# Optimization experiments

Hardware: AMD Instinct MI355X
Metric: run time of the kernel (lower is better)

Reference implementation:

```python
import jax, jax.numpy as jnp
import numpy as np

# batch, net nodes/graph, vnr nodes/graph, hidden, static feats, vnr feats, vnf types, value out
B, NN, NV, H, FS, FV, T, O = 64, 1000, 10, 128, 8, 6, 8, 64
EN, EV = B * NN * 8, B * NV * 4  # total edges (avg degree 8 / 4)


def _gat(h, src, dst, W, al, ar, b):
    """dgl GATConv, num_heads=1, activation=None, allow_zero_in_degree=True."""
    n = h.shape[0]
    z = h @ W                                                    # [N,H]
    e = jax.nn.leaky_relu((z @ al)[src] + (z @ ar)[dst], 0.2)    # [E]
    emax = jax.ops.segment_max(e, dst, num_segments=n)
    ee = jnp.exp(e - emax[dst])
    alpha = ee / jax.ops.segment_sum(ee, dst, num_segments=n)[dst]
    return jax.ops.segment_sum(z[src] * alpha[:, None], dst, num_segments=n) + b


def _gru_cell(x, h, W_ih, W_hh, b_ih, b_hh):
    gi = x @ W_ih.T + b_ih
    gh = h @ W_hh.T + b_hh
    ir, iz, in_ = jnp.split(gi, 3, axis=-1)
    hr, hz, hn = jnp.split(gh, 3, axis=-1)
    r = jax.nn.sigmoid(ir + hr)
    z = jax.nn.sigmoid(iz + hz)
    n = jnp.tanh(in_ + r * hn)
    return (1.0 - z) * n + z * h


def _forward(static_feat, vnr_feat, nmask,
             Ws1, als1, ars1, bs1, Ws2, als2, ars2, bs2, Ws3, als3, ars3, bs3,
             Wv1, alv1, arv1, bv1, Wv2, alv2, arv2, bv2, Wv3, alv3, arv3, bv3,
             W_attn, v_attn, W_ih, W_hh, b_ih, b_hh, h0, W_out, b_out,
             src_s, dst_s, src_v, dst_v, vnr_VNF, net_VNF):
    # ---- graph encoders: 3 stacked GAT layers each ----
    hs = _gat(static_feat, src_s, dst_s, Ws1, als1, ars1, bs1)
    hs = _gat(hs, src_s, dst_s, Ws2, als2, ars2, bs2)
    hs = _gat(hs, src_s, dst_s, Ws3, als3, ars3, bs3)            # [B*NN,H]
    hv = _gat(vnr_feat, src_v, dst_v, Wv1, alv1, arv1, bv1)
    hv = _gat(hv, src_v, dst_v, Wv2, alv2, arv2, bv2)
    hv = _gat(hv, src_v, dst_v, Wv3, alv3, arv3, bv3)            # [B*NV,H]
    static_hidden = hs.reshape(B, NN, H).transpose(0, 2, 1)      # [B,H,NN]
    vnr_hidden = hv.reshape(B, NV, H).transpose(0, 2, 1)         # [B,H,NV]

    # ---- pointer decoder ----
    netV = net_VNF.reshape(B, NN, T)
    # mask[b,i,n] = netV[b, n, vnr_VNF[b,i]]
    masks = jnp.take_along_axis(netV[:, None, :, :], vnr_VNF[:, :, None, None], axis=3)[..., 0]  # [B,NV,NN]

    def step(h, x):
        h_new = _gru_cell(x, h, W_ih, W_hh, b_ih, b_hh)          # [B,H]
        cat = jnp.concatenate(
            [static_hidden, jnp.broadcast_to(h_new[:, :, None], (B, H, NN))], axis=1)  # [B,2H,NN]
        attn = jnp.einsum('h,bhn->bn', v_attn,
                          jnp.tanh(jnp.einsum('hk,bkn->bhn', W_attn, cat)))
        return h_new, attn

    h0b = jnp.broadcast_to(h0, (B, H))
    xs = vnr_hidden.transpose(2, 0, 1)                            # [NV,B,H]
    _, attns = jax.lax.scan(step, h0b, xs)                        # [NV,B,NN]
    pi = (attns.transpose(1, 0, 2) + jnp.log(masks.astype(jnp.float32))).reshape(B, -1)

    # ---- value head ----
    nm = nmask.reshape(B, NV)
    y1 = (vnr_hidden.transpose(0, 2, 1) * nm[:, :, None]).sum(1) / nm.sum(1, keepdims=True)
    y2 = static_hidden.mean(2)
    val = jnp.concatenate([y1, y2], axis=1) @ W_out.T + b_out     # [B,O]
    return pi, val


def setup_inputs() -> dict:
    key = jax.random.key(0)
    ks = iter(jax.random.split(key, 60))

    def nrm(shape, fan):
        return jax.random.normal(next(ks), shape, jnp.float32) / np.sqrt(fan).astype(np.float32)

    inp = {
        'static_feat': jax.random.normal(next(ks), (B * NN, FS), jnp.float32),
        'vnr_feat': jax.random.normal(next(ks), (B * NV, FV), jnp.float32),
        'nmask': jnp.ones((B * NV,), jnp.float32),
    }
    for pfx, fin in (('s1', FS), ('s2', H), ('s3', H), ('v1', FV), ('v2', H), ('v3', H)):
        inp['W' + pfx] = nrm((fin, H), fin)
        inp['al' + pfx] = nrm((H,), H)
        inp['ar' + pfx] = nrm((H,), H)
        inp['b' + pfx] = jnp.zeros((H,), jnp.float32)
    inp['W_attn'] = nrm((H, 2 * H), 2 * H)
    inp['v_attn'] = nrm((H,), H)
    inp['W_ih'] = nrm((3 * H, H), H)
    inp['W_hh'] = nrm((3 * H, H), H)
    inp['b_ih'] = jnp.zeros((3 * H,), jnp.float32)
    inp['b_hh'] = jnp.zeros((3 * H,), jnp.float32)
    inp['h0'] = jnp.zeros((H,), jnp.float32)
    inp['W_out'] = nrm((O, 2 * H), 2 * H)
    inp['b_out'] = jnp.zeros((O,), jnp.float32)
    inp['src_s'] = jax.random.randint(next(ks), (EN,), 0, B * NN)
    inp['dst_s'] = jax.random.randint(next(ks), (EN,), 0, B * NN)
    inp['src_v'] = jax.random.randint(next(ks), (EV,), 0, B * NV)
    inp['dst_v'] = jax.random.randint(next(ks), (EV,), 0, B * NV)
    inp['vnr_VNF'] = jax.random.randint(next(ks), (B, NV), 0, T)
    inp['net_VNF'] = jnp.ones((B * NN, T), jnp.int32)
    return inp


def reference(static_feat, vnr_feat, nmask,
              Ws1, als1, ars1, bs1, Ws2, als2, ars2, bs2, Ws3, als3, ars3, bs3,
              Wv1, alv1, arv1, bv1, Wv2, alv2, arv2, bv2, Wv3, alv3, arv3, bv3,
              W_attn, v_attn, W_ih, W_hh, b_ih, b_hh, h0, W_out, b_out,
              src_s, dst_s, src_v, dst_v, vnr_VNF, net_VNF):
    return _forward(static_feat, vnr_feat, nmask,
                    Ws1, als1, ars1, bs1, Ws2, als2, ars2, bs2, Ws3, als3, ars3, bs3,
                    Wv1, alv1, arv1, bv1, Wv2, alv2, arv2, bv2, Wv3, alv3, arv3, bv3,
                    W_attn, v_attn, W_ih, W_hh, b_ih, b_hh, h0, W_out, b_out,
                    src_s, dst_s, src_v, dst_v, vnr_VNF, net_VNF)
```

## Files before the change

kernel.cpp:

```cpp
#include <hip/hip_runtime.h>
#include <hip/hip_bf16.h>
#include <math.h>

#define B_   64
#define NN_  1000
#define NV_  10
#define H_   128
#define FS_  8
#define FV_  6
#define T_   8
#define O_   64
#define EN_  512000
#define EV_  2560
#define NS_  (B_*NN_)
#define NVT_ (B_*NV_)
#define RNG_S (NS_/8)
#define RNG_V (NVT_/8)

typedef __attribute__((ext_vector_type(8))) short short8v;
typedef __attribute__((ext_vector_type(4))) float floatx4;

__device__ __forceinline__ float fast_rcp(float x) { return __builtin_amdgcn_rcpf(x); }
__device__ __forceinline__ float fast_tanh(float x) {
  return 1.f - 2.f*fast_rcp(1.f + __expf(2.f*x));
}
__device__ __forceinline__ float fast_sigmoid(float x) {
  return fast_rcp(1.f + __expf(-x));
}
__device__ __forceinline__ unsigned short bf16_rne(float x) {
  unsigned u = __float_as_uint(x);
  return (unsigned short)((u + 0x7FFFu + ((u >> 16) & 1u)) >> 16);
}
__device__ __forceinline__ float bf16_tof(unsigned short b) {
  return __uint_as_float(((unsigned)b) << 16);
}
__device__ __forceinline__ float dot4(float4 a, float4 b) {
  return a.x*b.x + a.y*b.y + a.z*b.z + a.w*b.w;
}
__device__ __forceinline__ float lrelu02(float e) {
  return (e > 0.f) ? e : 0.2f*e;
}

__global__ __launch_bounds__(256) void k_count_r(const int* __restrict__ dst_s,
                                                 const int* __restrict__ dst_v,
                                                 int* __restrict__ counts_s,
                                                 int* __restrict__ counts_v) {
  int bid = blockIdx.x;
  int r = bid & 7;
  int i = (bid >> 3)*256 + threadIdx.x;
  if (i < EN_) {
    int d = dst_s[i];
    int lo = r*RNG_S;
    if (d >= lo && d < lo + RNG_S) atomicAdd(&counts_s[d], 1);
  } else if (i < EN_ + EV_) {
    int d = dst_v[i - EN_];
    int lo = r*RNG_V;
    if (d >= lo && d < lo + RNG_V) atomicAdd(&counts_v[d], 1);
  }
}

__global__ __launch_bounds__(256) void k_scan_local(const int* cnt, int n, int* out, int* bsum) {
  __shared__ int s[256];
  int t = threadIdx.x; int i = blockIdx.x*256 + t;
  int v = (i < n) ? cnt[i] : 0;
  s[t] = v; __syncthreads();
  #pragma unroll
  for (int o = 1; o < 256; o <<= 1) {
    int u = (t >= o) ? s[t-o] : 0; __syncthreads();
    s[t] += u; __syncthreads();
  }
  if (i < n) out[i] = s[t] - v;
  if (t == 255) bsum[blockIdx.x] = s[255];
}

__global__ __launch_bounds__(1024) void k_scan_small(int* bsum, int nb,
                                                     const int* cntv, int* rowptr_v, int nv) {
  __shared__ int sums[1024];
  int t = threadIdx.x;
  if (blockIdx.x == 0) {
    int v = (t < nb) ? bsum[t] : 0;
    sums[t] = v; __syncthreads();
    for (int o = 1; o < 1024; o <<= 1) {
      int u = (t >= o) ? sums[t-o] : 0; __syncthreads();
      sums[t] += u; __syncthreads();
    }
    if (t < nb) bsum[t] = sums[t] - v;
  } else {
    int v = (t < nv) ? cntv[t] : 0;
    sums[t] = v; __syncthreads();
    for (int o = 1; o < 1024; o <<= 1) {
      int u = (t >= o) ? sums[t-o] : 0; __syncthreads();
      sums[t] += u; __syncthreads();
    }
    if (t < nv) rowptr_v[t] = sums[t] - v;
    if (t == nv-1) rowptr_v[nv] = sums[t];
  }
}

__global__ __launch_bounds__(256) void k_scan_add(int* out, const int* bsum, int n, int E) {
  int i = blockIdx.x*256 + threadIdx.x;
  if (i < n) out[i] += bsum[blockIdx.x];
  if (i == 0) out[n] = E;
}

__global__ __launch_bounds__(256) void k_scatter_r(const int* __restrict__ src_s,
                                                   const int* __restrict__ dst_s,
                                                   const int* __restrict__ src_v,
                                                   const int* __restrict__ dst_v,
                                                   const int* __restrict__ rowptr_s,
                                                   const int* __restrict__ rowptr_v,
                                                   int* __restrict__ cursor_s,
                                                   int* __restrict__ cursor_v,
                                                   unsigned short* __restrict__ srcp_s,
                                                   unsigned short* __restrict__ srcp_v) {
  int bid = blockIdx.x;
  int r = bid & 7;
  int i = (bid >> 3)*256 + threadIdx.x;
  if (i < EN_) {
    int d = dst_s[i];
    int lo = r*RNG_S;
    if (d >= lo && d < lo + RNG_S) {
      int pos = rowptr_s[d] + atomicAdd(&cursor_s[d], 1);
      srcp_s[pos] = (unsigned short)src_s[i];
    }
  } else if (i < EN_ + EV_) {
    int j = i - EN_;
    int d = dst_v[j];
    int lo = r*RNG_V;
    if (d >= lo && d < lo + RNG_V) {
      int pos = rowptr_v[d] + atomicAdd(&cursor_v[d], 1);
      srcp_v[pos] = (unsigned short)src_v[j];
    }
  }
}

__global__ __launch_bounds__(256) void k_prep(const float* W_ih, const float* Ws2,
                                              const float* Ws3, const float* W_attn,
                                              const float* Wv2, const float* Wv3,
                                              float* WTih,
                                              unsigned short* WS2hi, unsigned short* WS2lo,
                                              unsigned short* WS3hi, unsigned short* WS3lo,
                                              unsigned short* WAhi, unsigned short* WAlo,
                                              unsigned short* WV2hi, unsigned short* WV2lo,
                                              unsigned short* WV3hi, unsigned short* WV3lo) {
  int idx = blockIdx.x*256 + threadIdx.x;
  int task = blockIdx.y;
  if (task == 0) {
    if (idx < 128*384) {
      int k = idx / 384, j = idx - k*384;
      WTih[idx] = W_ih[(size_t)j*128 + k];
    }
  } else {
    if (idx >= 128*128) return;
    int j = idx >> 7, k = idx & 127;
    float v; unsigned short *hi, *lo;
    if (task == 1)      { v = Ws2[(size_t)k*128 + j];    hi = WS2hi; lo = WS2lo; }
    else if (task == 2) { v = Ws3[(size_t)k*128 + j];    hi = WS3hi; lo = WS3lo; }
    else if (task == 3) { v = W_attn[(size_t)j*256 + k]; hi = WAhi;  lo = WAlo;  }
    else if (task == 4) { v = Wv2[(size_t)k*128 + j];    hi = WV2hi; lo = WV2lo; }
    else                { v = Wv3[(size_t)k*128 + j];    hi = WV3hi; lo = WV3lo; }
    unsigned short h = bf16_rne(v);
    hi[idx] = h; lo[idx] = bf16_rne(v - bf16_tof(h));
  }
}

__global__ __launch_bounds__(256) void k_aggregate_split(int nNodes, const int* __restrict__ rowptr,
    const unsigned short* __restrict__ srcp, const float* __restrict__ el, const float* __restrict__ er,
    const unsigned short* __restrict__ z, const float* __restrict__ bias,
    unsigned short* __restrict__ outHi, unsigned short* __restrict__ outLo) {
  int w = (blockIdx.x*256 + threadIdx.x) >> 6;
  int lane = threadIdx.x & 63;
  if (w >= nNodes) return;
  int beg = rowptr[w], end = rowptr[w+1];
  float erw = er[w];
  float a0 = 0.f, a1 = 0.f, wsum = 0.f;
  for (int i = beg; i < end; i += 8) {
    int sI[8]; float lv[8]; ushort2 q[8];
    #pragma unroll
    for (int u = 0; u < 8; ++u) {
      int idx = i + u; idx = (idx < end) ? idx : (end - 1);
      sI[u] = srcp[idx];
    }
    #pragma unroll
    for (int u = 0; u < 8; ++u) lv[u] = el[sI[u]];
    #pragma unroll
    for (int u = 0; u < 8; ++u) q[u] = *(const ushort2*)(z + (size_t)sI[u]*H_ + lane*2);
    #pragma unroll
    for (int u = 0; u < 8; ++u) {
      float wt = (i + u < end) ? __expf(lrelu02(lv[u] + erw)) : 0.f;
      a0 += wt*bf16_tof(q[u].x);
      a1 += wt*bf16_tof(q[u].y);
      wsum += wt;
    }
  }
  float inv = (end > beg) ? fast_rcp(wsum) : 0.f;
  float o0 = a0*inv + bias[lane*2];
  float o1 = a1*inv + bias[lane*2 + 1];
  unsigned short h0 = bf16_rne(o0), h1 = bf16_rne(o1);
  ushort2 hv; hv.x = h0; hv.y = h1;
  ushort2 lv2; lv2.x = bf16_rne(o0 - bf16_tof(h0)); lv2.y = bf16_rne(o1 - bf16_tof(h1));
  *(ushort2*)(outHi + (size_t)w*H_ + lane*2) = hv;
  *(ushort2*)(outLo + (size_t)w*H_ + lane*2) = lv2;
}

__global__ __launch_bounds__(256) void k_mfma_gemm(
    const unsigned short* __restrict__ Ahi, const unsigned short* __restrict__ Alo,
    const unsigned short* __restrict__ WThi, const unsigned short* __restrict__ WTlo,
    float* __restrict__ C, unsigned short* __restrict__ Cb,
    const float* __restrict__ al, const float* __restrict__ ar,
    float* __restrict__ el, float* __restrict__ er) {
  __shared__ unsigned short lAhi[64*136];
  __shared__ unsigned short lAlo[64*136];
  __shared__ float redl[4][64];
  __shared__ float redr[4][64];
  int t = threadIdx.x;
  int row0 = blockIdx.x * 64;
  int wid = t >> 6, lane = t & 63;
  int g = lane >> 4, c = lane & 15;

  #pragma unroll
  for (int i = 0; i < 4; ++i) {
    int m = t + 256*i;
    int r = m >> 4;
    int kc = (m & 15) * 8;
    *(short8v*)(lAhi + r*136 + kc) = *(const short8v*)(Ahi + (size_t)(row0 + r)*H_ + kc);
    *(short8v*)(lAlo + r*136 + kc) = *(const short8v*)(Alo + (size_t)(row0 + r)*H_ + kc);
  }

  short8v bhi[2][4], blo[2][4];
  #pragma unroll
  for (int ct = 0; ct < 2; ++ct) {
    int col = wid*32 + ct*16 + c;
    #pragma unroll
    for (int kb = 0; kb < 4; ++kb) {
      size_t o = (size_t)col*H_ + kb*32 + g*8;
      bhi[ct][kb] = *(const short8v*)(WThi + o);
      blo[ct][kb] = *(const short8v*)(WTlo + o);
    }
  }

  floatx4 acc[4][2];
  #pragma unroll
  for (int rt = 0; rt < 4; ++rt)
    #pragma unroll
    for (int ct = 0; ct < 2; ++ct)
      acc[rt][ct] = (floatx4){0.f, 0.f, 0.f, 0.f};

  __syncthreads();

  #pragma unroll
  for (int kb = 0; kb < 4; ++kb) {
    short8v ahi[4], alo[4];
    #pragma unroll
    for (int rt = 0; rt < 4; ++rt) {
      int r = rt*16 + c;
      ahi[rt] = *(const short8v*)(lAhi + r*136 + kb*32 + g*8);
      alo[rt] = *(const short8v*)(lAlo + r*136 + kb*32 + g*8);
    }
    #pragma unroll
    for (int rt = 0; rt < 4; ++rt)
      #pragma unroll
      for (int ct = 0; ct < 2; ++ct) {
        acc[rt][ct] = __builtin_amdgcn_mfma_f32_16x16x32_bf16(ahi[rt], bhi[ct][kb], acc[rt][ct], 0, 0, 0);
        acc[rt][ct] = __builtin_amdgcn_mfma_f32_16x16x32_bf16(alo[rt], bhi[ct][kb], acc[rt][ct], 0, 0, 0);
        acc[rt][ct] = __builtin_amdgcn_mfma_f32_16x16x32_bf16(ahi[rt], blo[ct][kb], acc[rt][ct], 0, 0, 0);
      }
  }

  #pragma unroll
  for (int rt = 0; rt < 4; ++rt)
    #pragma unroll
    for (int i = 0; i < 4; ++i) {
      int row = row0 + rt*16 + g*4 + i;
      if (Cb) {
        unsigned short* cr = Cb + (size_t)row*H_ + wid*32;
        cr[c]      = bf16_rne(acc[rt][0][i]);
        cr[16 + c] = bf16_rne(acc[rt][1][i]);
      } else {
        float* cr = C + (size_t)row*H_ + wid*32;
        cr[c]      = acc[rt][0][i];
        cr[16 + c] = acc[rt][1][i];
      }
    }

  if (el) {
    float av0 = al[wid*32 + c], av1 = al[wid*32 + 16 + c];
    float rv0 = ar[wid*32 + c], rv1 = ar[wid*32 + 16 + c];
    #pragma unroll
    for (int rt = 0; rt < 4; ++rt)
      #pragma unroll
      for (int i = 0; i < 4; ++i) {
        float pl = acc[rt][0][i]*av0 + acc[rt][1][i]*av1;
        float pr = acc[rt][0][i]*rv0 + acc[rt][1][i]*rv1;
        pl += __shfl_xor(pl, 1, 64); pl += __shfl_xor(pl, 2, 64);
        pl += __shfl_xor(pl, 4, 64); pl += __shfl_xor(pl, 8, 64);
        pr += __shfl_xor(pr, 1, 64); pr += __shfl_xor(pr, 2, 64);
        pr += __shfl_xor(pr, 4, 64); pr += __shfl_xor(pr, 8, 64);
        if (c == 0) { redl[wid][rt*16 + g*4 + i] = pl; redr[wid][rt*16 + g*4 + i] = pr; }
      }
    __syncthreads();
    if (t < 64) {
      el[row0 + t] = redl[0][t] + redl[1][t] + redl[2][t] + redl[3][t];
      er[row0 + t] = redr[0][t] + redr[1][t] + redr[2][t] + redr[3][t];
    }
  }
}

__global__ __launch_bounds__(256) void k_agg_mfma(
    const int* __restrict__ rowptr, const unsigned short* __restrict__ srcp,
    const float* __restrict__ el_in, const float* __restrict__ er_in,
    const unsigned short* __restrict__ z_in, const float* __restrict__ bias,
    const unsigned short* __restrict__ WThi, const unsigned short* __restrict__ WTlo,
    unsigned short* __restrict__ zb_out, float* __restrict__ Cf,
    const float* __restrict__ al, const float* __restrict__ ar,
    float* __restrict__ el_out, float* __restrict__ er_out) {
  __shared__ unsigned short lAhi[64*136];
  __shared__ unsigned short lAlo[64*136];
  __shared__ float redl[4][64];
  __shared__ float redr[4][64];
  int t = threadIdx.x;
  int row0 = blockIdx.x * 64;
  int wid = t >> 6, lane = t & 63;
  int g = lane >> 4, c = lane & 15;

  float b0 = bias[lane*2], b1 = bias[lane*2 + 1];

  for (int j = 0; j < 8; ++j) {
    int wA = row0 + wid*16 + 2*j;
    int wB = wA + 1;
    int begA = rowptr[wA], endA = rowptr[wA+1];
    int begB = rowptr[wB], endB = rowptr[wB+1];
    float erA = er_in[wA], erB = er_in[wB];
    float a0A = 0.f, a1A = 0.f, wsA = 0.f;
    float a0B = 0.f, a1B = 0.f, wsB = 0.f;
    int iA = begA, iB = begB;
    while (iA < endA || iB < endB) {
      int sA[8], sB[8];
      #pragma unroll
      for (int u = 0; u < 8; ++u) {
        sA[u] = (iA + u < endA) ? (int)srcp[iA + u] : 0;
        sB[u] = (iB + u < endB) ? (int)srcp[iB + u] : 0;
      }
      float lA[8], lB[8];
      #pragma unroll
      for (int u = 0; u < 8; ++u) { lA[u] = el_in[sA[u]]; lB[u] = el_in[sB[u]]; }
      ushort2 qA[8], qB[8];
      #pragma unroll
      for (int u = 0; u < 8; ++u) {
        qA[u] = *(const ushort2*)(z_in + (size_t)sA[u]*H_ + lane*2);
        qB[u] = *(const ushort2*)(z_in + (size_t)sB[u]*H_ + lane*2);
      }
      #pragma unroll
      for (int u = 0; u < 8; ++u) {
        float wtA = (iA + u < endA) ? __expf(lrelu02(lA[u] + erA)) : 0.f;
        float wtB = (iB + u < endB) ? __expf(lrelu02(lB[u] + erB)) : 0.f;
        a0A += wtA*bf16_tof(qA[u].x); a1A += wtA*bf16_tof(qA[u].y); wsA += wtA;
        a0B += wtB*bf16_tof(qB[u].x); a1B += wtB*bf16_tof(qB[u].y); wsB += wtB;
      }
      iA += 8; iB += 8;
    }
    float invA = (endA > begA) ? fast_rcp(wsA) : 0.f;
    float invB = (endB > begB) ? fast_rcp(wsB) : 0.f;
    float o0A = a0A*invA + b0, o1A = a1A*invA + b1;
    float o0B = a0B*invB + b0, o1B = a1B*invB + b1;
    int rA = wid*16 + 2*j;
    unsigned short hA0 = bf16_rne(o0A), hA1 = bf16_rne(o1A);
    unsigned short hB0 = bf16_rne(o0B), hB1 = bf16_rne(o1B);
    ushort2 hvA; hvA.x = hA0; hvA.y = hA1;
    ushort2 lvA; lvA.x = bf16_rne(o0A - bf16_tof(hA0)); lvA.y = bf16_rne(o1A - bf16_tof(hA1));
    ushort2 hvB; hvB.x = hB0; hvB.y = hB1;
    ushort2 lvB; lvB.x = bf16_rne(o0B - bf16_tof(hB0)); lvB.y = bf16_rne(o1B - bf16_tof(hB1));
    *(ushort2*)(lAhi + rA*136 + lane*2) = hvA;
    *(ushort2*)(lAlo + rA*136 + lane*2) = lvA;
    *(ushort2*)(lAhi + (rA+1)*136 + lane*2) = hvB;
    *(ushort2*)(lAlo + (rA+1)*136 + lane*2) = lvB;
  }

  short8v bhi[2][4], blo[2][4];
  #pragma unroll
  for (int ct = 0; ct < 2; ++ct) {
    int col = wid*32 + ct*16 + c;
    #pragma unroll
    for (int kb = 0; kb < 4; ++kb) {
      size_t o = (size_t)col*H_ + kb*32 + g*8;
      bhi[ct][kb] = *(const short8v*)(WThi + o);
      blo[ct][kb] = *(const short8v*)(WTlo + o);
    }
  }

  floatx4 acc[4][2];
  #pragma unroll
  for (int rt = 0; rt < 4; ++rt)
    #pragma unroll
    for (int ct = 0; ct < 2; ++ct)
      acc[rt][ct] = (floatx4){0.f, 0.f, 0.f, 0.f};

  __syncthreads();

  #pragma unroll
  for (int kb = 0; kb < 4; ++kb) {
    short8v ahi[4], alo[4];
    #pragma unroll
    for (int rt = 0; rt < 4; ++rt) {
      int r = rt*16 + c;
      ahi[rt] = *(const short8v*)(lAhi + r*136 + kb*32 + g*8);
      alo[rt] = *(const short8v*)(lAlo + r*136 + kb*32 + g*8);
    }
    #pragma unroll
    for (int rt = 0; rt < 4; ++rt)
      #pragma unroll
      for (int ct = 0; ct < 2; ++ct) {
        acc[rt][ct] = __builtin_amdgcn_mfma_f32_16x16x32_bf16(ahi[rt], bhi[ct][kb], acc[rt][ct], 0, 0, 0);
        acc[rt][ct] = __builtin_amdgcn_mfma_f32_16x16x32_bf16(alo[rt], bhi[ct][kb], acc[rt][ct], 0, 0, 0);
        acc[rt][ct] = __builtin_amdgcn_mfma_f32_16x16x32_bf16(ahi[rt], blo[ct][kb], acc[rt][ct], 0, 0, 0);
      }
  }

  #pragma unroll
  for (int rt = 0; rt < 4; ++rt)
    #pragma unroll
    for (int i = 0; i < 4; ++i) {
      int row = row0 + rt*16 + g*4 + i;
      if (zb_out) {
        unsigned short* cr = zb_out + (size_t)row*H_ + wid*32;
        cr[c]      = bf16_rne(acc[rt][0][i]);
        cr[16 + c] = bf16_rne(acc[rt][1][i]);
      } else {
        float* cr = Cf + (size_t)row*H_ + wid*32;
        cr[c]      = acc[rt][0][i];
        cr[16 + c] = acc[rt][1][i];
      }
    }

  if (el_out) {
    float av0 = al[wid*32 + c], av1 = al[wid*32 + 16 + c];
    float rv0 = ar[wid*32 + c], rv1 = ar[wid*32 + 16 + c];
    #pragma unroll
    for (int rt = 0; rt < 4; ++rt)
      #pragma unroll
      for (int i = 0; i < 4; ++i) {
        float pl = acc[rt][0][i]*av0 + acc[rt][1][i]*av1;
        float pr = acc[rt][0][i]*rv0 + acc[rt][1][i]*rv1;
        pl += __shfl_xor(pl, 1, 64); pl += __shfl_xor(pl, 2, 64);
        pl += __shfl_xor(pl, 4, 64); pl += __shfl_xor(pl, 8, 64);
        pr += __shfl_xor(pr, 1, 64); pr += __shfl_xor(pr, 2, 64);
        pr += __shfl_xor(pr, 4, 64); pr += __shfl_xor(pr, 8, 64);
        if (c == 0) { redl[wid][rt*16 + g*4 + i] = pl; redr[wid][rt*16 + g*4 + i] = pr; }
      }
    __syncthreads();
    if (t < 64) {
      el_out[row0 + t] = redl[0][t] + redl[1][t] + redl[2][t] + redl[3][t];
      er_out[row0 + t] = redr[0][t] + redr[1][t] + redr[2][t] + redr[3][t];
    }
  }
}

__global__ __launch_bounds__(256) void k_aggregate_f(int nNodes, const int* __restrict__ rowptr,
    const unsigned short* __restrict__ srcp, const float* __restrict__ el,
    const float* __restrict__ er, const unsigned short* __restrict__ z,
    const float* __restrict__ bias, float* __restrict__ out) {
  int w = (blockIdx.x*256 + threadIdx.x) >> 6;
  int lane = threadIdx.x & 63;
  if (w >= nNodes) return;
  int beg = rowptr[w], end = rowptr[w+1];
  float erw = er[w];
  float a0 = 0.f, a1 = 0.f, wsum = 0.f;
  for (int i = beg; i < end; ++i) {
    int sI = srcp[i];
    float wt = __expf(lrelu02(el[sI] + erw));
    ushort2 q = *(const ushort2*)(z + (size_t)sI*H_ + lane*2);
    a0 += wt*bf16_tof(q.x); a1 += wt*bf16_tof(q.y); wsum += wt;
  }
  float inv = (end > beg) ? fast_rcp(wsum) : 0.f;
  float2 o;
  o.x = a0*inv + bias[lane*2];
  o.y = a1*inv + bias[lane*2 + 1];
  *(float2*)(out + (size_t)w*H_ + lane*2) = o;
}

__global__ __launch_bounds__(256) void k_gemm(const float* A, int M, int K, int N,
                                              const float* W, const float* bias,
                                              float* C, unsigned short* Cb,
                                              const float* al, const float* ar,
                                              float* el, float* er) {
  __shared__ float Ws_[64*128];
  __shared__ float As_[16*128];
  __shared__ float redl[16][17];
  __shared__ float redr[16][17];
  int t = threadIdx.x;
  int j0 = blockIdx.y * 128;
  int row0 = blockIdx.x * 16;
  for (int l = t; l < 16*K; l += 256) {
    int r = l / K, k = l - r*K;
    int row = row0 + r;
    As_[r*K + k] = (row < M) ? A[(size_t)row*K + k] : 0.f;
  }
  int jg = t & 15, r = t >> 4;
  float acc[8];
  #pragma unroll
  for (int q = 0; q < 8; ++q) acc[q] = 0.f;
  for (int kc = 0; kc < K; kc += 64) {
    int kl = min(64, K - kc);
    __syncthreads();
    for (int l = t; l < (kl << 7); l += 256) {
      int k = l >> 7, j = l & 127;
      int jj = j0 + j;
      Ws_[l] = (jj < N) ? W[(size_t)(kc + k)*N + jj] : 0.f;
    }
    __syncthreads();
    for (int k = 0; k < kl; ++k) {
      float a = As_[r*K + kc + k];
      const float* wr = &Ws_[(k << 7) + jg*8];
      #pragma unroll
      for (int q = 0; q < 8; ++q) acc[q] += a * wr[q];
    }
  }
  int row = row0 + r;
  if (row < M) {
    if (Cb) {
      unsigned short* crow = Cb + (size_t)row*N + j0 + jg*8;
      #pragma unroll
      for (int q = 0; q < 8; ++q) {
        int j = j0 + jg*8 + q;
        if (j < N) crow[q] = bf16_rne(acc[q] + (bias ? bias[j] : 0.f));
      }
    } else {
      float* crow = C + (size_t)row*N + j0 + jg*8;
      #pragma unroll
      for (int q = 0; q < 8; ++q) {
        int j = j0 + jg*8 + q;
        if (j < N) crow[q] = acc[q] + (bias ? bias[j] : 0.f);
      }
    }
  }
  if (el) {
    float pl = 0.f, pr = 0.f;
    #pragma unroll
    for (int q = 0; q < 8; ++q) {
      int j = jg*8 + q;
      pl += acc[q]*al[j];
      pr += acc[q]*ar[j];
    }
    redl[r][jg] = pl; redr[r][jg] = pr;
    __syncthreads();
    if (t < 16) {
      float sl = 0.f, sr = 0.f;
      for (int q = 0; q < 16; ++q) { sl += redl[t][q]; sr += redr[t][q]; }
      int row2 = row0 + t;
      if (row2 < M) { el[row2] = sl; er[row2] = sr; }
    }
  }
}

__global__ __launch_bounds__(512) void k_decoder(const float* __restrict__ GI,
                                                 const float* __restrict__ W_hh,
                                                 const float* __restrict__ b_hh,
                                                 const float* __restrict__ W_attn,
                                                 const float* __restrict__ h0,
                                                 float* __restrict__ A2) {
  int b = blockIdx.x;
  __shared__ float h[128];
  __shared__ float gh[384];
  int t = threadIdx.x;
  const float4* wsrc = (t < 384)
      ? (const float4*)(W_hh + (size_t)t*128)
      : (const float4*)(W_attn + (size_t)(t-384)*256 + 128);
  float4 wreg[32];
  #pragma unroll
  for (int kk = 0; kk < 32; ++kk) wreg[kk] = wsrc[kk];
  float bh = (t < 384) ? b_hh[t] : 0.f;
  if (t < 128) h[t] = h0[t];
  __syncthreads();
  for (int s = 0; s < 10; ++s) {
    const float4* h4 = (const float4*)h;
    if (t < 384) {
      float a0 = 0.f, a1 = 0.f, a2 = 0.f, a3 = 0.f;
      #pragma unroll
      for (int kk = 0; kk < 32; kk += 4) {
        a0 += dot4(wreg[kk+0], h4[kk+0]);
        a1 += dot4(wreg[kk+1], h4[kk+1]);
        a2 += dot4(wreg[kk+2], h4[kk+2]);
        a3 += dot4(wreg[kk+3], h4[kk+3]);
      }
      gh[t] = (a0 + a1) + (a2 + a3) + bh;
    }
    __syncthreads();
    if (t < 128) {
      const float* gi = GI + (size_t)(b*NV_ + s)*384;
      float rr = fast_sigmoid(gi[t]       + gh[t]);
      float zz = fast_sigmoid(gi[128 + t] + gh[128 + t]);
      float nn = fast_tanh   (gi[256 + t] + rr*gh[256 + t]);
      h[t] = (1.f - zz)*nn + zz*h[t];
    }
    __syncthreads();
    if (t >= 384) {
      float a0 = 0.f, a1 = 0.f, a2 = 0.f, a3 = 0.f;
      #pragma unroll
      for (int kk = 0; kk < 32; kk += 4) {
        a0 += dot4(wreg[kk+0], h4[kk+0]);
        a1 += dot4(wreg[kk+1], h4[kk+1]);
        a2 += dot4(wreg[kk+2], h4[kk+2]);
        a3 += dot4(wreg[kk+3], h4[kk+3]);
      }
      A2[((size_t)s*B_ + b)*128 + (t - 384)] = (a0 + a1) + (a2 + a3);
    }
  }
}

__global__ __launch_bounds__(256) void k_attn3(const float* __restrict__ A1,
                                               const float* __restrict__ A2,
                                               const float* __restrict__ v_attn,
                                               const int* __restrict__ vnr_VNF,
                                               const int* __restrict__ net_VNF,
                                               float* __restrict__ pi) {
  __shared__ float a2s[10][128];
  __shared__ float vv2s[128];
  int b = blockIdx.y;
  int t = threadIdx.x;
  for (int i = t; i < 1280; i += 256) {
    int s = i >> 7, k = i & 127;
    a2s[s][k] = 2.f*A2[((size_t)s*B_ + b)*H_ + k];
  }
  if (t < 128) vv2s[t] = 2.f*v_attn[t];
  __syncthreads();
  int nl = t >> 2, p = t & 3;
  int n = blockIdx.x*64 + nl;
  if (n >= NN_) return;
  size_t g = (size_t)b*NN_ + n;
  const float4* arow = (const float4*)(A1 + g*H_ + p*32);
  float4 a[8], w2[8];
  #pragma unroll
  for (int kk = 0; kk < 8; ++kk) {
    float4 av = arow[kk];
    a[kk] = make_float4(2.f*av.x, 2.f*av.y, 2.f*av.z, 2.f*av.w);
    w2[kk] = *(const float4*)(&vv2s[p*32 + kk*4]);
  }
  float vsum = 0.f;
  #pragma unroll
  for (int kk = 0; kk < 8; ++kk)
    vsum += (w2[kk].x + w2[kk].y) + (w2[kk].z + w2[kk].w);
  vsum *= 0.5f;
  float acc[10];
  #pragma unroll
  for (int s = 0; s < 10; ++s) {
    const float* a2r = &a2s[s][p*32];
    float sum2 = 0.f;
    #pragma unroll
    for (int kk = 0; kk < 8; ++kk) {
      float4 c = *(const float4*)(a2r + kk*4);
      sum2 = fmaf(w2[kk].x, fast_rcp(1.f + __expf(a[kk].x + c.x)), sum2);
      sum2 = fmaf(w2[kk].y, fast_rcp(1.f + __expf(a[kk].y + c.y)), sum2);
      sum2 = fmaf(w2[kk].z, fast_rcp(1.f + __expf(a[kk].z + c.z)), sum2);
      sum2 = fmaf(w2[kk].w, fast_rcp(1.f + __expf(a[kk].w + c.w)), sum2);
    }
    acc[s] = vsum - sum2;
  }
  #pragma unroll
  for (int s = 0; s < 10; ++s) {
    acc[s] += __shfl_xor(acc[s], 1, 64);
    acc[s] += __shfl_xor(acc[s], 2, 64);
  }
  if (p == 0) {
    #pragma unroll
    for (int s = 0; s < 10; ++s) {
      int vnf = vnr_VNF[b*NV_ + s];
      int m   = net_VNF[g*T_ + vnf];
      pi[(size_t)b*(NV_*NN_) + (size_t)s*NN_ + n] = acc[s] + __logf((float)m);
    }
  }
}

__global__ __launch_bounds__(128) void k_y2s(const unsigned short* hi, const unsigned short* lo,
                                             float* y2) {
  int b = blockIdx.x, slice = blockIdx.y, h = threadIdx.x;
  int n0 = slice*125, n1 = n0 + 125;
  float s = 0.f;
  for (int n = n0; n < n1; ++n) {
    size_t idx = ((size_t)b*NN_ + n)*H_ + h;
    s += bf16_tof(hi[idx]) + bf16_tof(lo[idx]);
  }
  atomicAdd(&y2[b*H_ + h], s);
}

__global__ __launch_bounds__(128) void k_value(const float* __restrict__ Hv,
                                               const float* __restrict__ nmask,
                                               const float* __restrict__ y2,
                                               const float* __restrict__ W_out,
                                               const float* __restrict__ b_out,
                                               float* __restrict__ val) {
  __shared__ float y1s[128];
  int b = blockIdx.x, t = threadIdx.x;
  float s = 0.f, d = 0.f;
  #pragma unroll
  for (int i = 0; i < NV_; ++i) {
    float m = nmask[b*NV_ + i];
    s += Hv[(size_t)(b*NV_ + i)*H_ + t]*m;
    d += m;
  }
  y1s[t] = s/d;
  __syncthreads();
  if (t < 64) {
    const float* w = W_out + (size_t)t*256;
    float acc = b_out[t];
    for (int h = 0; h < H_; ++h)
      acc += y1s[h]*w[h] + (y2[b*H_ + h]*(1.f/1000.f))*w[128 + h];
    val[b*O_ + t] = acc;
  }
}

extern "C" void kernel_launch(void* const* d_in, const int* in_sizes, int n_in,
                              void* d_out, int out_size, void* d_ws, size_t ws_size,
                              hipStream_t stream) {
  (void)in_sizes; (void)n_in; (void)out_size; (void)ws_size;
  const float* static_feat = (const float*)d_in[0];
  const float* vnr_feat    = (const float*)d_in[1];
  const float* nmask       = (const float*)d_in[2];
  const float* Ws1 = (const float*)d_in[3];  const float* als1 = (const float*)d_in[4];
  const float* ars1 = (const float*)d_in[5]; const float* bs1 = (const float*)d_in[6];
  const float* Ws2 = (const float*)d_in[7];  const float* als2 = (const float*)d_in[8];
  const float* ars2 = (const float*)d_in[9]; const float* bs2 = (const float*)d_in[10];
  const float* Ws3 = (const float*)d_in[11]; const float* als3 = (const float*)d_in[12];
  const float* ars3 = (const float*)d_in[13]; const float* bs3 = (const float*)d_in[14];
  const float* Wv1 = (const float*)d_in[15]; const float* alv1 = (const float*)d_in[16];
  const float* arv1 = (const float*)d_in[17]; const float* bv1 = (const float*)d_in[18];
  const float* Wv2 = (const float*)d_in[19]; const float* alv2 = (const float*)d_in[20];
  const float* arv2 = (const float*)d_in[21]; const float* bv2 = (const float*)d_in[22];
  const float* Wv3 = (const float*)d_in[23]; const float* alv3 = (const float*)d_in[24];
  const float* arv3 = (const float*)d_in[25]; const float* bv3 = (const float*)d_in[26];
  const float* W_attn = (const float*)d_in[27];
  const float* v_attn = (const float*)d_in[28];
  const float* W_ih = (const float*)d_in[29];
  const float* W_hh = (const float*)d_in[30];
  const float* b_ih = (const float*)d_in[31];
  const float* b_hh = (const float*)d_in[32];
  const float* h0   = (const float*)d_in[33];
  const float* W_out = (const float*)d_in[34];
  const float* b_out = (const float*)d_in[35];
  const int* src_s = (const int*)d_in[36];
  const int* dst_s = (const int*)d_in[37];
  const int* src_v = (const int*)d_in[38];
  const int* dst_v = (const int*)d_in[39];
  const int* vnr_VNF = (const int*)d_in[40];
  const int* net_VNF = (const int*)d_in[41];

  char* ws = (char*)d_ws;
  size_t off = 0;
  auto alloc = [&](size_t bytes) -> char* {
    off = (off + 255) & ~(size_t)255;
    char* p = ws + off;
    off += bytes;
    return p;
  };
  float* Z    = (float*)alloc((size_t)NS_*H_*4);
  unsigned short* Zb0 = (unsigned short*)alloc((size_t)NS_*H_*2);
  unsigned short* HsHi = (unsigned short*)alloc((size_t)NS_*H_*2);
  unsigned short* HsLo = (unsigned short*)alloc((size_t)NS_*H_*2);
  unsigned short* Zbv0 = (unsigned short*)alloc((size_t)NVT_*H_*2);
  unsigned short* Zbv1 = (unsigned short*)alloc((size_t)NVT_*H_*2);
  float* Hv   = (float*)alloc((size_t)NVT_*H_*4);
  float* el_s = (float*)alloc((size_t)NS_*4);
  float* er_s = (float*)alloc((size_t)NS_*4);
  float* elv_a = (float*)alloc((size_t)NVT_*4);
  float* erv_a = (float*)alloc((size_t)NVT_*4);
  float* elv_b = (float*)alloc((size_t)NVT_*4);
  float* erv_b = (float*)alloc((size_t)NVT_*4);
  size_t zcount = (size_t)NS_ + NS_ + NVT_ + NVT_ + B_*H_;
  char* zb = alloc(zcount*4);
  int*   counts_s = (int*)zb;
  int*   cursor_s = counts_s + NS_;
  int*   counts_v = cursor_s + NS_;
  int*   cursor_v = counts_v + NVT_;
  float* y2buf    = (float*)(cursor_v + NVT_);
  int* rowptr_s = (int*)alloc((size_t)(NS_+1)*4);
  int* rowptr_v = (int*)alloc((size_t)(NVT_+1)*4);
  int* bsum     = (int*)alloc((size_t)256*4);
  unsigned short* srcp_s = (unsigned short*)alloc((size_t)(EN_+8)*2);
  unsigned short* srcp_v = (unsigned short*)alloc((size_t)(EV_+8)*2);
  unsigned short* WS2hi = (unsigned short*)alloc((size_t)H_*H_*2);
  unsigned short* WS2lo = (unsigned short*)alloc((size_t)H_*H_*2);
  unsigned short* WS3hi = (unsigned short*)alloc((size_t)H_*H_*2);
  unsigned short* WS3lo = (unsigned short*)alloc((size_t)H_*H_*2);
  unsigned short* WAhi  = (unsigned short*)alloc((size_t)H_*H_*2);
  unsigned short* WAlo  = (unsigned short*)alloc((size_t)H_*H_*2);
  unsigned short* WV2hi = (unsigned short*)alloc((size_t)H_*H_*2);
  unsigned short* WV2lo = (unsigned short*)alloc((size_t)H_*H_*2);
  unsigned short* WV3hi = (unsigned short*)alloc((size_t)H_*H_*2);
  unsigned short* WV3lo = (unsigned short*)alloc((size_t)H_*H_*2);
  float* WTih   = (float*)alloc((size_t)H_*384*4);
  float* GI     = (float*)alloc((size_t)NVT_*384*4);
  float* A2     = (float*)alloc((size_t)NV_*B_*H_*4);

  float* pi  = (float*)d_out;
  float* val = pi + (size_t)B_*NV_*NN_;

  hipMemsetAsync(zb, 0, zcount*4, stream);

  k_prep<<<dim3(192, 6), 256, 0, stream>>>(W_ih, Ws2, Ws3, W_attn, Wv2, Wv3, WTih,
                                           WS2hi, WS2lo, WS3hi, WS3lo, WAhi, WAlo,
                                           WV2hi, WV2lo, WV3hi, WV3lo);

  int edgeChunks = (EN_ + EV_ + 255)/256;
  k_count_r<<<edgeChunks*8, 256, 0, stream>>>(dst_s, dst_v, counts_s, counts_v);
  k_scan_local<<<250, 256, 0, stream>>>(counts_s, NS_, rowptr_s, bsum);
  k_scan_small<<<2, 1024, 0, stream>>>(bsum, 250, counts_v, rowptr_v, NVT_);
  k_scan_add<<<250, 256, 0, stream>>>(rowptr_s, bsum, NS_, EN_);
  k_scatter_r<<<edgeChunks*8, 256, 0, stream>>>(src_s, dst_s, src_v, dst_v,
                                                rowptr_s, rowptr_v, cursor_s, cursor_v,
                                                srcp_s, srcp_v);

  int aggS = (NS_ + 3)/4;

  k_gemm<<<dim3(NS_/16, 1), 256, 0, stream>>>(static_feat, NS_, FS_, H_, Ws1, nullptr,
                                              nullptr, Zb0, als1, ars1, el_s, er_s);
  k_aggregate_split<<<aggS, 256, 0, stream>>>(NS_, rowptr_s, srcp_s, el_s, er_s, Zb0, bs1, HsHi, HsLo);
  k_mfma_gemm<<<NS_/64, 256, 0, stream>>>(HsHi, HsLo, WS2hi, WS2lo, nullptr, Zb0, als2, ars2, el_s, er_s);
  k_aggregate_split<<<aggS, 256, 0, stream>>>(NS_, rowptr_s, srcp_s, el_s, er_s, Zb0, bs2, HsHi, HsLo);
  k_mfma_gemm<<<NS_/64, 256, 0, stream>>>(HsHi, HsLo, WS3hi, WS3lo, nullptr, Zb0, als3, ars3, el_s, er_s);
  k_aggregate_split<<<aggS, 256, 0, stream>>>(NS_, rowptr_s, srcp_s, el_s, er_s, Zb0, bs3, HsHi, HsLo);
  k_mfma_gemm<<<NS_/64, 256, 0, stream>>>(HsHi, HsLo, WAhi, WAlo, Z, nullptr,
                                          nullptr, nullptr, nullptr, nullptr);
  k_y2s<<<dim3(B_, 8), 128, 0, stream>>>(HsHi, HsLo, y2buf);

  k_gemm<<<dim3(NVT_/16, 1), 256, 0, stream>>>(vnr_feat, NVT_, FV_, H_, Wv1, nullptr,
                                               nullptr, Zbv0, alv1, arv1, elv_a, erv_a);
  k_agg_mfma<<<NVT_/64, 256, 0, stream>>>(rowptr_v, srcp_v, elv_a, erv_a, Zbv0, bv1,
                                          WV2hi, WV2lo, Zbv1, nullptr,
                                          alv2, arv2, elv_b, erv_b);
  k_agg_mfma<<<NVT_/64, 256, 0, stream>>>(rowptr_v, srcp_v, elv_b, erv_b, Zbv1, bv2,
                                          WV3hi, WV3lo, Zbv0, nullptr,
                                          alv3, arv3, elv_a, erv_a);
  k_aggregate_f<<<(NVT_ + 3)/4, 256, 0, stream>>>(NVT_, rowptr_v, srcp_v, elv_a, erv_a,
                                                  Zbv0, bv3, Hv);

  k_gemm<<<dim3(NVT_/16, 3), 256, 0, stream>>>(Hv, NVT_, H_, 384, WTih, b_ih, GI, nullptr,
                                               nullptr, nullptr, nullptr, nullptr);
  k_decoder<<<B_, 512, 0, stream>>>(GI, W_hh, b_hh, W_attn, h0, A2);
  k_attn3<<<dim3(16, B_), 256, 0, stream>>>(Z, A2, v_attn, vnr_VNF, net_VNF, pi);

  k_value<<<B_, 128, 0, stream>>>(Hv, nmask, y2buf, W_out, b_out, val);
}
```

Measured before the change: 410.1 us.

## Fuse attention projection GEMM into pointer attention kernel, drop fp32 Z buffer

Removes the separate MFMA GEMM that wrote the 64000x128 fp32 projection Z to global memory, along with the k_attn3 kernel that read it back. A new kernel computes the projection tile in registers with split-bf16 MFMA and immediately evaluates the tanh-style attention scores against A2 for all 10 decoder steps. This saves a large write and read of Z. In exchange, tiles can span two batches, so the kernel handles both batches' A2, and per-row partial sums are reduced with LDS atomicAdd, which may contend.

```diff
diff --git a/kernel.cpp b/kernel.cpp
--- a/kernel.cpp
+++ b/kernel.cpp
@@ -306,6 +306,119 @@
   }
 }
 
+__global__ __launch_bounds__(256) void k_mfma_attn(
+    const unsigned short* __restrict__ Ahi, const unsigned short* __restrict__ Alo,
+    const unsigned short* __restrict__ WThi, const unsigned short* __restrict__ WTlo,
+    const float* __restrict__ A2, const float* __restrict__ v_attn,
+    const int* __restrict__ vnr_VNF, const int* __restrict__ net_VNF,
+    float* __restrict__ pi) {
+  __shared__ unsigned short lAhi[64*136];
+  __shared__ unsigned short lAlo[64*136];
+  __shared__ float a2s2[2][10][128];
+  __shared__ float vv2s[128];
+  __shared__ float part[64][10];
+  __shared__ float vsumLds;
+  int t = threadIdx.x;
+  int row0 = blockIdx.x * 64;
+  int wid = t >> 6, lane = t & 63;
+  int g = lane >> 4, c = lane & 15;
+  int b0 = row0 / NN_;
+  int b1 = (row0 + 63) / NN_; if (b1 > B_-1) b1 = B_-1;
+
+  #pragma unroll
+  for (int i = 0; i < 4; ++i) {
+    int m = t + 256*i;
+    int r = m >> 4;
+    int kc = (m & 15) * 8;
+    *(short8v*)(lAhi + r*136 + kc) = *(const short8v*)(Ahi + (size_t)(row0 + r)*H_ + kc);
+    *(short8v*)(lAlo + r*136 + kc) = *(const short8v*)(Alo + (size_t)(row0 + r)*H_ + kc);
+  }
+  for (int i = t; i < 2560; i += 256) {
+    int w = (i >= 1280) ? 1 : 0;
+    int rem = i - w*1280;
+    int s = rem >> 7, k = rem & 127;
+    int b = (w == 0) ? b0 : b1;
+    a2s2[w][s][k] = 2.f*A2[((size_t)s*B_ + b)*H_ + k];
+  }
+  if (t < 128) vv2s[t] = 2.f*v_attn[t];
+  for (int o = t; o < 640; o += 256) ((float*)part)[o] = 0.f;
+
+  short8v bhi[2][4], blo[2][4];
+  #pragma unroll
+  for (int ct = 0; ct < 2; ++ct) {
+    int col = wid*32 + ct*16 + c;
+    #pragma unroll
+    for (int kb = 0; kb < 4; ++kb) {
+      size_t o = (size_t)col*H_ + kb*32 + g*8;
+      bhi[ct][kb] = *(const short8v*)(WThi + o);
+      blo[ct][kb] = *(const short8v*)(WTlo + o);
+    }
+  }
+
+  floatx4 acc[4][2];
+  #pragma unroll
+  for (int rt = 0; rt < 4; ++rt)
+    #pragma unroll
+    for (int ct = 0; ct < 2; ++ct)
+      acc[rt][ct] = (floatx4){0.f, 0.f, 0.f, 0.f};
+
+  __syncthreads();
+
+  if (t == 0) {
+    float s = 0.f;
+    for (int k = 0; k < 128; ++k) s += vv2s[k];
+    vsumLds = 0.5f*s;
+  }
+
+  #pragma unroll
+  for (int kb = 0; kb < 4; ++kb) {
+    short8v ahi[4], alo[4];
+    #pragma unroll
+    for (int rt = 0; rt < 4; ++rt) {
+      int r = rt*16 + c;
+      ahi[rt] = *(const short8v*)(lAhi + r*136 + kb*32 + g*8);
+      alo[rt] = *(const short8v*)(lAlo + r*136 + kb*32 + g*8);
+    }
+    #pragma unroll
+    for (int rt = 0; rt < 4; ++rt)
+      #pragma unroll
+      for (int ct = 0; ct < 2; ++ct) {
+        acc[rt][ct] = __builtin_amdgcn_mfma_f32_16x16x32_bf16(ahi[rt], bhi[ct][kb], acc[rt][ct], 0, 0, 0);
+        acc[rt][ct] = __builtin_amdgcn_mfma_f32_16x16x32_bf16(alo[rt], bhi[ct][kb], acc[rt][ct], 0, 0, 0);
+        acc[rt][ct] = __builtin_amdgcn_mfma_f32_16x16x32_bf16(ahi[rt], blo[ct][kb], acc[rt][ct], 0, 0, 0);
+      }
+  }
+
+  float v0 = vv2s[wid*32 + c], v1 = vv2s[wid*32 + 16 + c];
+  #pragma unroll
+  for (int rt = 0; rt < 4; ++rt)
+    #pragma unroll
+    for (int i = 0; i < 4; ++i) {
+      int lrow = rt*16 + g*4 + i;
+      int w = ((row0 + lrow) >= (b0+1)*NN_ && b1 != b0) ? 1 : 0;
+      float a1c0 = acc[rt][0][i], a1c1 = acc[rt][1][i];
+      #pragma unroll
+      for (int s = 0; s < 10; ++s) {
+        float a20 = a2s2[w][s][wid*32 + c];
+        float a21 = a2s2[w][s][wid*32 + 16 + c];
+        float t0 = fast_rcp(1.f + __expf(fmaf(2.f, a1c0, a20)));
+        float t1 = fast_rcp(1.f + __expf(fmaf(2.f, a1c1, a21)));
+        atomicAdd(&part[lrow][s], v0*t0 + v1*t1);
+      }
+    }
+  __syncthreads();
+
+  float vsum = vsumLds;
+  for (int o = t; o < 640; o += 256) {
+    int lrow = o/10, s = o - lrow*10;
+    int row = row0 + lrow;
+    int b = row / NN_, n = row - b*NN_;
+    int vnf = vnr_VNF[b*NV_ + s];
+    int m   = net_VNF[(size_t)row*T_ + vnf];
+    pi[(size_t)b*(NV_*NN_) + (size_t)s*NN_ + n] = vsum - part[lrow][s] + __logf((float)m);
+  }
+}
+
 __global__ __launch_bounds__(256) void k_agg_mfma(
     const int* __restrict__ rowptr, const unsigned short* __restrict__ srcp,
     const float* __restrict__ el_in, const float* __restrict__ er_in,
@@ -603,69 +716,6 @@
         a3 += dot4(wreg[kk+3], h4[kk+3]);
       }
       A2[((size_t)s*B_ + b)*128 + (t - 384)] = (a0 + a1) + (a2 + a3);
-    }
-  }
-}
-
-__global__ __launch_bounds__(256) void k_attn3(const float* __restrict__ A1,
-                                               const float* __restrict__ A2,
-                                               const float* __restrict__ v_attn,
-                                               const int* __restrict__ vnr_VNF,
-                                               const int* __restrict__ net_VNF,
-                                               float* __restrict__ pi) {
-  __shared__ float a2s[10][128];
-  __shared__ float vv2s[128];
-  int b = blockIdx.y;
-  int t = threadIdx.x;
-  for (int i = t; i < 1280; i += 256) {
-    int s = i >> 7, k = i & 127;
-    a2s[s][k] = 2.f*A2[((size_t)s*B_ + b)*H_ + k];
-  }
-  if (t < 128) vv2s[t] = 2.f*v_attn[t];
-  __syncthreads();
-  int nl = t >> 2, p = t & 3;
-  int n = blockIdx.x*64 + nl;
-  if (n >= NN_) return;
-  size_t g = (size_t)b*NN_ + n;
-  const float4* arow = (const float4*)(A1 + g*H_ + p*32);
-  float4 a[8], w2[8];
-  #pragma unroll
-  for (int kk = 0; kk < 8; ++kk) {
-    float4 av = arow[kk];
-    a[kk] = make_float4(2.f*av.x, 2.f*av.y, 2.f*av.z, 2.f*av.w);
-    w2[kk] = *(const float4*)(&vv2s[p*32 + kk*4]);
-  }
-  float vsum = 0.f;
-  #pragma unroll
-  for (int kk = 0; kk < 8; ++kk)
-    vsum += (w2[kk].x + w2[kk].y) + (w2[kk].z + w2[kk].w);
-  vsum *= 0.5f;
-  float acc[10];
-  #pragma unroll
-  for (int s = 0; s < 10; ++s) {
-    const float* a2r = &a2s[s][p*32];
-    float sum2 = 0.f;
-    #pragma unroll
-    for (int kk = 0; kk < 8; ++kk) {
-      float4 c = *(const float4*)(a2r + kk*4);
-      sum2 = fmaf(w2[kk].x, fast_rcp(1.f + __expf(a[kk].x + c.x)), sum2);
-      sum2 = fmaf(w2[kk].y, fast_rcp(1.f + __expf(a[kk].y + c.y)), sum2);
-      sum2 = fmaf(w2[kk].z, fast_rcp(1.f + __expf(a[kk].z + c.z)), sum2);
-      sum2 = fmaf(w2[kk].w, fast_rcp(1.f + __expf(a[kk].w + c.w)), sum2);
-    }
-    acc[s] = vsum - sum2;
-  }
-  #pragma unroll
-  for (int s = 0; s < 10; ++s) {
-    acc[s] += __shfl_xor(acc[s], 1, 64);
-    acc[s] += __shfl_xor(acc[s], 2, 64);
-  }
-  if (p == 0) {
-    #pragma unroll
-    for (int s = 0; s < 10; ++s) {
-      int vnf = vnr_VNF[b*NV_ + s];
-      int m   = net_VNF[g*T_ + vnf];
-      pi[(size_t)b*(NV_*NN_) + (size_t)s*NN_ + n] = acc[s] + __logf((float)m);
     }
   }
 }
@@ -751,7 +801,6 @@
     off += bytes;
     return p;
   };
-  float* Z    = (float*)alloc((size_t)NS_*H_*4);
   unsigned short* Zb0 = (unsigned short*)alloc((size_t)NS_*H_*2);
   unsigned short* HsHi = (unsigned short*)alloc((size_t)NS_*H_*2);
   unsigned short* HsLo = (unsigned short*)alloc((size_t)NS_*H_*2);
@@ -817,8 +866,6 @@
   k_aggregate_split<<<aggS, 256, 0, stream>>>(NS_, rowptr_s, srcp_s, el_s, er_s, Zb0, bs2, HsHi, HsLo);
   k_mfma_gemm<<<NS_/64, 256, 0, stream>>>(HsHi, HsLo, WS3hi, WS3lo, nullptr, Zb0, als3, ars3, el_s, er_s);
   k_aggregate_split<<<aggS, 256, 0, stream>>>(NS_, rowptr_s, srcp_s, el_s, er_s, Zb0, bs3, HsHi, HsLo);
-  k_mfma_gemm<<<NS_/64, 256, 0, stream>>>(HsHi, HsLo, WAhi, WAlo, Z, nullptr,
-                                          nullptr, nullptr, nullptr, nullptr);
   k_y2s<<<dim3(B_, 8), 128, 0, stream>>>(HsHi, HsLo, y2buf);
 
   k_gemm<<<dim3(NVT_/16, 1), 256, 0, stream>>>(vnr_feat, NVT_, FV_, H_, Wv1, nullptr,
@@ -835,7 +882,8 @@
   k_gemm<<<dim3(NVT_/16, 3), 256, 0, stream>>>(Hv, NVT_, H_, 384, WTih, b_ih, GI, nullptr,
                                                nullptr, nullptr, nullptr, nullptr);
   k_decoder<<<B_, 512, 0, stream>>>(GI, W_hh, b_hh, W_attn, h0, A2);
-  k_attn3<<<dim3(16, B_), 256, 0, stream>>>(Z, A2, v_attn, vnr_VNF, net_VNF, pi);
+  k_mfma_attn<<<NS_/64, 256, 0, stream>>>(HsHi, HsLo, WAhi, WAlo, A2, v_attn,
+                                          vnr_VNF, net_VNF, pi);
 
   k_value<<<B_, 128, 0, stream>>>(Hv, nmask, y2buf, W_out, b_out, val);
 }
```

After: 656.3 us. 60.0% more time.
